# Kernel optimization log

Hardware: AMD Instinct MI355X
Metric: run time of the kernel (lower is better)

The kernel has to match this reference:

```python
import jax, jax.numpy as jnp
import numpy as np

EPS = 1e-8

def _conv(x, w, b=None):
    # NCHW conv, stride 1, SAME padding (k=3, pad=1)
    y = jax.lax.conv_general_dilated(x, w, (1, 1), 'SAME',
                                     dimension_numbers=('NCHW', 'OIHW', 'NCHW'))
    if b is not None:
        y = y + b[None, :, None, None]
    return y

def setup_inputs() -> dict:
    key = jax.random.key(0)
    ks = jax.random.split(key, 6)
    B, C, H, W = 512, 1024, 8, 8
    return {
        'x': jax.random.normal(ks[0], (B, C, H, W), jnp.float32),
        'w1_1': jax.random.normal(ks[1], (1, 1, 3, 3), jnp.float32) * 0.1,
        'w5': jax.random.normal(ks[2], (4, 2, 3, 3), jnp.float32) * 0.1,
        'b5': jax.random.normal(ks[3], (4,), jnp.float32) * 0.1,
        'w6': jax.random.normal(ks[4], (1, 4, 3, 3), jnp.float32) * 0.1,
        'b6': jax.random.normal(ks[5], (1,), jnp.float32) * 0.1,
    }

def reference(x, w1_1, w5, b5, w6, b6):
    B, C, H, W = x.shape  # H == W == 8 by module construction
    m = jnp.max(x, axis=1, keepdims=True)  # [B,1,H,W] channel max
    # 2x2 non-overlapping windows, torch unfold layout -> [B,1,(H/2)*(W/2),4]
    win = m.reshape(B, 1, H // 2, 2, W // 2, 2)
    win = win.transpose(0, 1, 2, 4, 3, 5).reshape(B, 1, (H // 2) * (W // 2), 4)
    # probabilistic pooling: clean inf/nan/negatives, sample per window
    winc = jnp.where(jnp.isinf(win) | jnp.isnan(win) | (win < 0), EPS, win)
    skey = jax.random.key(1)
    idx = jax.random.categorical(skey, winc, axis=-1)  # softmax(winc) multinomial
    mo2 = jnp.take_along_axis(winc, idx[..., None], axis=-1)[..., 0]
    mo2 = mo2.reshape(B, 1, H // 2, W // 2)
    # adaptive max/avg pool (4,4) on 8x8 == 2x2 pooling, reuse windows
    mo3 = win.max(axis=-1).reshape(B, 1, H // 2, W // 2)
    ao4 = win.mean(axis=-1).reshape(B, 1, H // 2, W // 2)
    out2 = 0.1 * mo2 + 0.6 * mo3 + 0.3 * ao4
    out2 = _conv(out2, w1_1)  # bias-free 1->1 conv
    out2 = jax.image.resize(out2, (B, 1, H, W), method='bilinear')  # align_corners=False
    out1 = jnp.concatenate([m, out2], axis=1)  # [B,2,H,W]
    gate = jax.nn.sigmoid(_conv(jax.nn.relu(_conv(out1, w5, b5)), w6, b6))  # [B,1,H,W]
    return jax.nn.relu(x * gate)
```

## Files before the change

kernel.cpp:

```cpp
#include <hip/hip_runtime.h>
#include <math.h>

#define C_DIM 1024
#define HW 64
#define NT 1024
#define F4_PER_BATCH 16384
#define PER_T 16
#define EPSV 1e-8f
#define TINYF 1.17549435e-38f

typedef float f32x4_t __attribute__((ext_vector_type(4)));

__device__ __forceinline__ void keepf(float& v) { asm volatile("" : "+v"(v)); }
__device__ __forceinline__ void keep4(float4& v) {
    keepf(v.x); keepf(v.y); keepf(v.z); keepf(v.w);
}

__device__ __forceinline__ void threefry2x32_01(unsigned x0, unsigned x1,
                                                unsigned& o0, unsigned& o1) {
    const unsigned ks0 = 0u, ks1 = 1u, ks2 = 0x1BD11BDBu;
    x0 += ks0; x1 += ks1;
#define TF_R(r) { x0 += x1; x1 = (x1 << (r)) | (x1 >> (32 - (r))); x1 ^= x0; }
    TF_R(13) TF_R(15) TF_R(26) TF_R(6)
    x0 += ks1; x1 += ks2 + 1u;
    TF_R(17) TF_R(29) TF_R(16) TF_R(24)
    x0 += ks2; x1 += ks0 + 2u;
    TF_R(13) TF_R(15) TF_R(26) TF_R(6)
    x0 += ks0; x1 += ks1 + 3u;
    TF_R(17) TF_R(29) TF_R(16) TF_R(24)
    x0 += ks1; x1 += ks2 + 4u;
    TF_R(13) TF_R(15) TF_R(26) TF_R(6)
    x0 += ks2; x1 += ks0 + 5u;
#undef TF_R
    o0 = x0; o1 = x1;
}

__device__ __forceinline__ unsigned jax_random_bits(unsigned n) {
    unsigned o0, o1;
    threefry2x32_01(0u, n, o0, o1);
    return o0 ^ o1;
}

__device__ __forceinline__ bool bad_val(float v) {
    return ((__float_as_uint(v) & 0x7F800000u) == 0x7F800000u) || (v < 0.0f);
}

__global__ __launch_bounds__(NT) void sa_fused_kernel(
    const float* __restrict__ x,
    const float* __restrict__ w11,
    const float* __restrict__ w5,
    const float* __restrict__ b5,
    const float* __restrict__ w6,
    const float* __restrict__ b6,
    float* __restrict__ out)
{
    const int b = blockIdx.x;
    const int t = threadIdx.x;

    const float4* __restrict__ xb = (const float4*)x + (size_t)b * F4_PER_BATCH;
    float4* __restrict__ ob = (float4*)out + (size_t)b * F4_PER_BATCH;

    __shared__ float4 red[16 * 16];
    __shared__ float sm[64];
    __shared__ float sa16[16];
    __shared__ float sb16[16];
    __shared__ float so2[64];
    __shared__ float shid[4 * 64];
    __shared__ __align__(16) float sgate[64];

    float4 xv[PER_T];
    float4 pm = make_float4(-INFINITY, -INFINITY, -INFINITY, -INFINITY);
#pragma unroll
    for (int i = 0; i < PER_T; ++i) {
        xv[i] = xb[t + NT * i];
        pm.x = fmaxf(pm.x, xv[i].x); pm.y = fmaxf(pm.y, xv[i].y);
        pm.z = fmaxf(pm.z, xv[i].z); pm.w = fmaxf(pm.w, xv[i].w);
    }
#pragma unroll
    for (int i = 0; i < PER_T; ++i) keep4(xv[i]);

#pragma unroll
    for (int off = 16; off <= 32; off <<= 1) {
        pm.x = fmaxf(pm.x, __shfl_xor(pm.x, off, 64));
        pm.y = fmaxf(pm.y, __shfl_xor(pm.y, off, 64));
        pm.z = fmaxf(pm.z, __shfl_xor(pm.z, off, 64));
        pm.w = fmaxf(pm.w, __shfl_xor(pm.w, off, 64));
    }
    const int wv = t >> 6, lane = t & 63;
    if (lane < 16) red[wv * 16 + lane] = pm;
    __syncthreads();

    if (t < 64) {
        {
            int g = t & 15, set = t >> 4;
            float4 a = red[(set * 4 + 0) * 16 + g];
#pragma unroll
            for (int w = 1; w < 4; ++w) {
                float4 o = red[(set * 4 + w) * 16 + g];
                a.x = fmaxf(a.x, o.x); a.y = fmaxf(a.y, o.y);
                a.z = fmaxf(a.z, o.z); a.w = fmaxf(a.w, o.w);
            }
#pragma unroll
            for (int off = 16; off <= 32; off <<= 1) {
                a.x = fmaxf(a.x, __shfl_xor(a.x, off, 64));
                a.y = fmaxf(a.y, __shfl_xor(a.y, off, 64));
                a.z = fmaxf(a.z, __shfl_xor(a.z, off, 64));
                a.w = fmaxf(a.w, __shfl_xor(a.w, off, 64));
            }
            if (t < 16) {
                sm[t * 4 + 0] = a.x; sm[t * 4 + 1] = a.y;
                sm[t * 4 + 2] = a.z; sm[t * 4 + 3] = a.w;
            }
        }
        __builtin_amdgcn_wave_barrier();

        {
            int w = t >> 2, j = t & 3;
            int hh = 2 * (w >> 2) + (j >> 1), ww = 2 * (w & 3) + (j & 1);
            float v = sm[hh * 8 + ww];
            float wc = bad_val(v) ? EPSV : v;
            unsigned bits = jax_random_bits((unsigned)(b * 64 + t));
            float f = __uint_as_float(0x3F800000u | (bits >> 9)) - 1.0f;
            float u = fmaxf(TINYF, f + TINYF);
            float sg = -logf(-logf(u));
            float s = wc + sg;
            int bi = j;
            float bwc = wc;
            float mx = v;
            float ssum = v;
#pragma unroll
            for (int m = 1; m <= 2; m <<= 1) {
                float s2   = __shfl_xor(s, m, 64);
                int   bi2  = __shfl_xor(bi, m, 64);
                float bwc2 = __shfl_xor(bwc, m, 64);
                float mx2  = __shfl_xor(mx, m, 64);
                float ss2  = __shfl_xor(ssum, m, 64);
                bool take = (s2 > s) || (s2 == s && bi2 < bi);
                if (take) { s = s2; bi = bi2; bwc = bwc2; }
                mx = fmaxf(mx, mx2);
                ssum += ss2;
            }
            if (j == 0) sa16[w] = 0.1f * bwc + 0.6f * mx + 0.3f * (ssum * 0.25f);
        }
        __builtin_amdgcn_wave_barrier();

        if (t < 16) {
            int i = t >> 2, j = t & 3;
            float acc = 0.0f;
#pragma unroll
            for (int dy = -1; dy <= 1; ++dy) {
                int yy = i + dy;
                if (yy < 0 || yy > 3) continue;
#pragma unroll
                for (int dx = -1; dx <= 1; ++dx) {
                    int xx = j + dx;
                    if (xx < 0 || xx > 3) continue;
                    acc += sa16[yy * 4 + xx] * w11[(dy + 1) * 3 + (dx + 1)];
                }
            }
            sb16[t] = acc;
        }
        __builtin_amdgcn_wave_barrier();

        {
            int y = t >> 3, xx2 = t & 7;
            float sy = (y + 0.5f) * 0.5f - 0.5f;
            float sx = (xx2 + 0.5f) * 0.5f - 0.5f;
            float fy = fminf(fmaxf(sy, 0.0f), 3.0f);
            float fx = fminf(fmaxf(sx, 0.0f), 3.0f);
            int iy0 = (int)floorf(fy); int iy1 = min(iy0 + 1, 3); float ry = fy - (float)iy0;
            int ix0 = (int)floorf(fx); int ix1 = min(ix0 + 1, 3); float rx = fx - (float)ix0;
            float v00 = sb16[iy0 * 4 + ix0], v01 = sb16[iy0 * 4 + ix1];
            float v10 = sb16[iy1 * 4 + ix0], v11 = sb16[iy1 * 4 + ix1];
            float top = v00 * (1.0f - rx) + v01 * rx;
            float bot = v10 * (1.0f - rx) + v11 * rx;
            so2[t] = top * (1.0f - ry) + bot * ry;
        }
        __builtin_amdgcn_wave_barrier();

        {
            int y = t >> 3, x2 = t & 7;
            float a0 = b5[0], a1 = b5[1], a2 = b5[2], a3 = b5[3];
#pragma unroll
            for (int dy = -1; dy <= 1; ++dy) {
                int yy = y + dy;
                if (yy < 0 || yy > 7) continue;
#pragma unroll
                for (int dx = -1; dx <= 1; ++dx) {
                    int xx = x2 + dx;
                    if (xx < 0 || xx > 7) continue;
                    float i0 = sm[yy * 8 + xx];
                    float i1 = so2[yy * 8 + xx];
                    int kk = (dy + 1) * 3 + (dx + 1);
                    a0 += i0 * w5[0 * 18 + kk] + i1 * w5[0 * 18 + 9 + kk];
                    a1 += i0 * w5[1 * 18 + kk] + i1 * w5[1 * 18 + 9 + kk];
                    a2 += i0 * w5[2 * 18 + kk] + i1 * w5[2 * 18 + 9 + kk];
                    a3 += i0 * w5[3 * 18 + kk] + i1 * w5[3 * 18 + 9 + kk];
                }
            }
            shid[0 * 64 + t] = fmaxf(a0, 0.0f);
            shid[1 * 64 + t] = fmaxf(a1, 0.0f);
            shid[2 * 64 + t] = fmaxf(a2, 0.0f);
            shid[3 * 64 + t] = fmaxf(a3, 0.0f);
        }
        __builtin_amdgcn_wave_barrier();

        {
            int y = t >> 3, x2 = t & 7;
            float acc = b6[0];
#pragma unroll
            for (int dy = -1; dy <= 1; ++dy) {
                int yy = y + dy;
                if (yy < 0 || yy > 7) continue;
#pragma unroll
                for (int dx = -1; dx <= 1; ++dx) {
                    int xx = x2 + dx;
                    if (xx < 0 || xx > 7) continue;
                    int kk = (dy + 1) * 3 + (dx + 1);
                    int p = yy * 8 + xx;
                    acc += shid[0 * 64 + p] * w6[0 + kk]
                         + shid[1 * 64 + p] * w6[9 + kk]
                         + shid[2 * 64 + p] * w6[18 + kk]
                         + shid[3 * 64 + p] * w6[27 + kk];
                }
            }
            sgate[t] = 1.0f / (1.0f + expf(-acc));
        }
    }
    __syncthreads();

    const float4 gv = ((const float4*)sgate)[t & 15];
#pragma unroll
    for (int i = 0; i < PER_T; ++i) {
        float4 v = xv[i];
        f32x4_t o;
        o.x = fmaxf(v.x * gv.x, 0.0f);
        o.y = fmaxf(v.y * gv.y, 0.0f);
        o.z = fmaxf(v.z * gv.z, 0.0f);
        o.w = fmaxf(v.w * gv.w, 0.0f);
        __builtin_nontemporal_store(o, (f32x4_t*)&ob[t + NT * i]);
    }
}

extern "C" void kernel_launch(void* const* d_in, const int* in_sizes, int n_in,
                              void* d_out, int out_size, void* d_ws, size_t ws_size,
                              hipStream_t stream) {
    const float* x   = (const float*)d_in[0];
    const float* w11 = (const float*)d_in[1];
    const float* w5  = (const float*)d_in[2];
    const float* b5  = (const float*)d_in[3];
    const float* w6  = (const float*)d_in[4];
    const float* b6  = (const float*)d_in[5];
    float* out  = (float*)d_out;

    int B = in_sizes[0] / (C_DIM * HW);
    sa_fused_kernel<<<dim3(B), dim3(NT), 0, stream>>>(x, w11, w5, b5, w6, b6, out);
}
```

Measured before the change: 243.2 us.

## Process two batches per block and overlap second load with first gate network

Each block now handles two batch items. The second batch's 64 KB load and its Gumbel noise generation are issued while the first batch's small gate network runs, and the first batch's Gumbel noise is computed while its own loads are in flight. In the write phase, x is reloaded from global memory (likely an L2 hit) instead of being held in registers, which cuts register pressure but adds reads. The grid is halved to B/2 blocks, which lowers parallelism and assumes B is even.

```diff
diff --git a/kernel.cpp b/kernel.cpp
--- a/kernel.cpp
+++ b/kernel.cpp
@@ -4,17 +4,14 @@
 #define C_DIM 1024
 #define HW 64
 #define NT 1024
-#define F4_PER_BATCH 16384
+#define F4B 16384
 #define PER_T 16
 #define EPSV 1e-8f
 #define TINYF 1.17549435e-38f
 
 typedef float f32x4_t __attribute__((ext_vector_type(4)));
 
-__device__ __forceinline__ void keepf(float& v) { asm volatile("" : "+v"(v)); }
-__device__ __forceinline__ void keep4(float4& v) {
-    keepf(v.x); keepf(v.y); keepf(v.z); keepf(v.w);
-}
+__device__ __forceinline__ void keepf(float v) { asm volatile("" :: "v"(v)); }
 
 __device__ __forceinline__ void threefry2x32_01(unsigned x0, unsigned x1,
                                                 unsigned& o0, unsigned& o1) {
@@ -41,8 +38,157 @@
     return o0 ^ o1;
 }
 
+__device__ __forceinline__ float gumbel01(unsigned n) {
+    unsigned bits = jax_random_bits(n);
+    float f = __uint_as_float(0x3F800000u | (bits >> 9)) - 1.0f;
+    float u = fmaxf(TINYF, f + TINYF);
+    return -logf(-logf(u));
+}
+
 __device__ __forceinline__ bool bad_val(float v) {
     return ((__float_as_uint(v) & 0x7F800000u) == 0x7F800000u) || (v < 0.0f);
+}
+
+__device__ __forceinline__ void middle_net(
+    int t, float sgum,
+    const float4* __restrict__ red,
+    const float* __restrict__ w11, const float* __restrict__ w5,
+    const float* __restrict__ b5, const float* __restrict__ w6,
+    const float* __restrict__ b6,
+    float* sm, float* sa16, float* sb16, float* so2, float* shid,
+    float* sgate)
+{
+    {
+        int g = t & 15, set = t >> 4;
+        float4 a = red[(set * 4 + 0) * 16 + g];
+#pragma unroll
+        for (int w = 1; w < 4; ++w) {
+            float4 o = red[(set * 4 + w) * 16 + g];
+            a.x = fmaxf(a.x, o.x); a.y = fmaxf(a.y, o.y);
+            a.z = fmaxf(a.z, o.z); a.w = fmaxf(a.w, o.w);
+        }
+#pragma unroll
+        for (int off = 16; off <= 32; off <<= 1) {
+            a.x = fmaxf(a.x, __shfl_xor(a.x, off, 64));
+            a.y = fmaxf(a.y, __shfl_xor(a.y, off, 64));
+            a.z = fmaxf(a.z, __shfl_xor(a.z, off, 64));
+            a.w = fmaxf(a.w, __shfl_xor(a.w, off, 64));
+        }
+        if (t < 16) {
+            sm[t * 4 + 0] = a.x; sm[t * 4 + 1] = a.y;
+            sm[t * 4 + 2] = a.z; sm[t * 4 + 3] = a.w;
+        }
+    }
+    __builtin_amdgcn_wave_barrier();
+
+    {
+        int w = t >> 2, j = t & 3;
+        int hh = 2 * (w >> 2) + (j >> 1), ww = 2 * (w & 3) + (j & 1);
+        float v = sm[hh * 8 + ww];
+        float wc = bad_val(v) ? EPSV : v;
+        float s = wc + sgum;
+        int bi = j;
+        float bwc = wc;
+        float mx = v;
+        float ssum = v;
+#pragma unroll
+        for (int m = 1; m <= 2; m <<= 1) {
+            float s2   = __shfl_xor(s, m, 64);
+            int   bi2  = __shfl_xor(bi, m, 64);
+            float bwc2 = __shfl_xor(bwc, m, 64);
+            float mx2  = __shfl_xor(mx, m, 64);
+            float ss2  = __shfl_xor(ssum, m, 64);
+            bool take = (s2 > s) || (s2 == s && bi2 < bi);
+            if (take) { s = s2; bi = bi2; bwc = bwc2; }
+            mx = fmaxf(mx, mx2);
+            ssum += ss2;
+        }
+        if (j == 0) sa16[w] = 0.1f * bwc + 0.6f * mx + 0.3f * (ssum * 0.25f);
+    }
+    __builtin_amdgcn_wave_barrier();
+
+    if (t < 16) {
+        int i = t >> 2, j = t & 3;
+        float acc = 0.0f;
+#pragma unroll
+        for (int dy = -1; dy <= 1; ++dy) {
+            int yy = i + dy;
+            if (yy < 0 || yy > 3) continue;
+#pragma unroll
+            for (int dx = -1; dx <= 1; ++dx) {
+                int xx = j + dx;
+                if (xx < 0 || xx > 3) continue;
+                acc += sa16[yy * 4 + xx] * w11[(dy + 1) * 3 + (dx + 1)];
+            }
+        }
+        sb16[t] = acc;
+    }
+    __builtin_amdgcn_wave_barrier();
+
+    {
+        int y = t >> 3, xx2 = t & 7;
+        float sy = (y + 0.5f) * 0.5f - 0.5f;
+        float sx = (xx2 + 0.5f) * 0.5f - 0.5f;
+        float fy = fminf(fmaxf(sy, 0.0f), 3.0f);
+        float fx = fminf(fmaxf(sx, 0.0f), 3.0f);
+        int iy0 = (int)floorf(fy); int iy1 = min(iy0 + 1, 3); float ry = fy - (float)iy0;
+        int ix0 = (int)floorf(fx); int ix1 = min(ix0 + 1, 3); float rx = fx - (float)ix0;
+        float v00 = sb16[iy0 * 4 + ix0], v01 = sb16[iy0 * 4 + ix1];
+        float v10 = sb16[iy1 * 4 + ix0], v11 = sb16[iy1 * 4 + ix1];
+        float top = v00 * (1.0f - rx) + v01 * rx;
+        float bot = v10 * (1.0f - rx) + v11 * rx;
+        so2[t] = top * (1.0f - ry) + bot * ry;
+    }
+    __builtin_amdgcn_wave_barrier();
+
+    {
+        int y = t >> 3, x2 = t & 7;
+        float a0 = b5[0], a1 = b5[1], a2 = b5[2], a3 = b5[3];
+#pragma unroll
+        for (int dy = -1; dy <= 1; ++dy) {
+            int yy = y + dy;
+            if (yy < 0 || yy > 7) continue;
+#pragma unroll
+            for (int dx = -1; dx <= 1; ++dx) {
+                int xx = x2 + dx;
+                if (xx < 0 || xx > 7) continue;
+                float i0 = sm[yy * 8 + xx];
+                float i1 = so2[yy * 8 + xx];
+                int kk = (dy + 1) * 3 + (dx + 1);
+                a0 += i0 * w5[0 * 18 + kk] + i1 * w5[0 * 18 + 9 + kk];
+                a1 += i0 * w5[1 * 18 + kk] + i1 * w5[1 * 18 + 9 + kk];
+                a2 += i0 * w5[2 * 18 + kk] + i1 * w5[2 * 18 + 9 + kk];
+                a3 += i0 * w5[3 * 18 + kk] + i1 * w5[3 * 18 + 9 + kk];
+            }
+        }
+        shid[0 * 64 + t] = fmaxf(a0, 0.0f);
+        shid[1 * 64 + t] = fmaxf(a1, 0.0f);
+        shid[2 * 64 + t] = fmaxf(a2, 0.0f);
+        shid[3 * 64 + t] = fmaxf(a3, 0.0f);
+    }
+    __builtin_amdgcn_wave_barrier();
+
+    {
+        int y = t >> 3, x2 = t & 7;
+        float acc = b6[0];
+#pragma unroll
+        for (int dy = -1; dy <= 1; ++dy) {
+            int yy = y + dy;
+            if (yy < 0 || yy > 7) continue;
+#pragma unroll
+            for (int dx = -1; dx <= 1; ++dx) {
+                int xx = x2 + dx;
+                if (xx < 0 || xx > 7) continue;
+                int kk = (dy + 1) * 3 + (dx + 1);
+                int p = yy * 8 + xx;
+                acc += shid[0 * 64 + p] * w6[0 + kk]
+                     + shid[1 * 64 + p] * w6[9 + kk]
+                     + shid[2 * 64 + p] * w6[18 + kk]
+                     + shid[3 * 64 + p] * w6[27 + kk];
+            }
+        }
+        sgate[t] = 1.0f / (1.0f + expf(-acc));
+    }
 }
 
 __global__ __launch_bounds__(NT) void sa_fused_kernel(
@@ -54,31 +200,38 @@
     const float* __restrict__ b6,
     float* __restrict__ out)
 {
-    const int b = blockIdx.x;
+    const int bid = blockIdx.x;
     const int t = threadIdx.x;
-
-    const float4* __restrict__ xb = (const float4*)x + (size_t)b * F4_PER_BATCH;
-    float4* __restrict__ ob = (float4*)out + (size_t)b * F4_PER_BATCH;
-
-    __shared__ float4 red[16 * 16];
-    __shared__ float sm[64];
-    __shared__ float sa16[16];
-    __shared__ float sb16[16];
-    __shared__ float so2[64];
-    __shared__ float shid[4 * 64];
-    __shared__ __align__(16) float sgate[64];
+    const int half = gridDim.x;
+    const int b0 = bid, b1 = bid + half;
+    const int wv = t >> 6, lane = t & 63;
+
+    const float4* __restrict__ x4 = (const float4*)x;
+    const float4* __restrict__ xb0 = x4 + (size_t)b0 * F4B;
+    const float4* __restrict__ xb1 = x4 + (size_t)b1 * F4B;
+    float4* __restrict__ ob0 = (float4*)out + (size_t)b0 * F4B;
+    float4* __restrict__ ob1 = (float4*)out + (size_t)b1 * F4B;
+
+    __shared__ float4 red0[16 * 16];
+    __shared__ float4 red1[16 * 16];
+    __shared__ float sm[64], sa16[16], sb16[16], so2[64], shid[4 * 64];
+    __shared__ __align__(16) float sgate0[64];
+    __shared__ __align__(16) float sgate1[64];
 
     float4 xv[PER_T];
+#pragma unroll
+    for (int i = 0; i < PER_T; ++i) xv[i] = xb0[t + NT * i];
+    if (t == 0) {
+        keepf(w11[0]); keepf(w5[0]); keepf(w5[32]); keepf(w5[64]);
+        keepf(b5[0]);  keepf(w6[0]); keepf(w6[32]); keepf(b6[0]);
+    }
+    const float sgum0 = gumbel01((unsigned)(b0 * 64 + lane));
     float4 pm = make_float4(-INFINITY, -INFINITY, -INFINITY, -INFINITY);
 #pragma unroll
     for (int i = 0; i < PER_T; ++i) {
-        xv[i] = xb[t + NT * i];
         pm.x = fmaxf(pm.x, xv[i].x); pm.y = fmaxf(pm.y, xv[i].y);
         pm.z = fmaxf(pm.z, xv[i].z); pm.w = fmaxf(pm.w, xv[i].w);
     }
-#pragma unroll
-    for (int i = 0; i < PER_T; ++i) keep4(xv[i]);
-
 #pragma unroll
     for (int off = 16; off <= 32; off <<= 1) {
         pm.x = fmaxf(pm.x, __shfl_xor(pm.x, off, 64));
@@ -86,159 +239,62 @@
         pm.z = fmaxf(pm.z, __shfl_xor(pm.z, off, 64));
         pm.w = fmaxf(pm.w, __shfl_xor(pm.w, off, 64));
     }
-    const int wv = t >> 6, lane = t & 63;
-    if (lane < 16) red[wv * 16 + lane] = pm;
+    if (lane < 16) red0[wv * 16 + lane] = pm;
     __syncthreads();
 
-    if (t < 64) {
-        {
-            int g = t & 15, set = t >> 4;
-            float4 a = red[(set * 4 + 0) * 16 + g];
-#pragma unroll
-            for (int w = 1; w < 4; ++w) {
-                float4 o = red[(set * 4 + w) * 16 + g];
-                a.x = fmaxf(a.x, o.x); a.y = fmaxf(a.y, o.y);
-                a.z = fmaxf(a.z, o.z); a.w = fmaxf(a.w, o.w);
-            }
-#pragma unroll
-            for (int off = 16; off <= 32; off <<= 1) {
-                a.x = fmaxf(a.x, __shfl_xor(a.x, off, 64));
-                a.y = fmaxf(a.y, __shfl_xor(a.y, off, 64));
-                a.z = fmaxf(a.z, __shfl_xor(a.z, off, 64));
-                a.w = fmaxf(a.w, __shfl_xor(a.w, off, 64));
-            }
-            if (t < 16) {
-                sm[t * 4 + 0] = a.x; sm[t * 4 + 1] = a.y;
-                sm[t * 4 + 2] = a.z; sm[t * 4 + 3] = a.w;
-            }
-        }
-        __builtin_amdgcn_wave_barrier();
-
-        {
-            int w = t >> 2, j = t & 3;
-            int hh = 2 * (w >> 2) + (j >> 1), ww = 2 * (w & 3) + (j & 1);
-            float v = sm[hh * 8 + ww];
-            float wc = bad_val(v) ? EPSV : v;
-            unsigned bits = jax_random_bits((unsigned)(b * 64 + t));
-            float f = __uint_as_float(0x3F800000u | (bits >> 9)) - 1.0f;
-            float u = fmaxf(TINYF, f + TINYF);
-            float sg = -logf(-logf(u));
-            float s = wc + sg;
-            int bi = j;
-            float bwc = wc;
-            float mx = v;
-            float ssum = v;
-#pragma unroll
-            for (int m = 1; m <= 2; m <<= 1) {
-                float s2   = __shfl_xor(s, m, 64);
-                int   bi2  = __shfl_xor(bi, m, 64);
-                float bwc2 = __shfl_xor(bwc, m, 64);
-                float mx2  = __shfl_xor(mx, m, 64);
-                float ss2  = __shfl_xor(ssum, m, 64);
-                bool take = (s2 > s) || (s2 == s && bi2 < bi);
-                if (take) { s = s2; bi = bi2; bwc = bwc2; }
-                mx = fmaxf(mx, mx2);
-                ssum += ss2;
-            }
-            if (j == 0) sa16[w] = 0.1f * bwc + 0.6f * mx + 0.3f * (ssum * 0.25f);
-        }
-        __builtin_amdgcn_wave_barrier();
-
-        if (t < 16) {
-            int i = t >> 2, j = t & 3;
-            float acc = 0.0f;
-#pragma unroll
-            for (int dy = -1; dy <= 1; ++dy) {
-                int yy = i + dy;
-                if (yy < 0 || yy > 3) continue;
-#pragma unroll
-                for (int dx = -1; dx <= 1; ++dx) {
-                    int xx = j + dx;
-                    if (xx < 0 || xx > 3) continue;
-                    acc += sa16[yy * 4 + xx] * w11[(dy + 1) * 3 + (dx + 1)];
-                }
-            }
-            sb16[t] = acc;
-        }
-        __builtin_amdgcn_wave_barrier();
-
-        {
-            int y = t >> 3, xx2 = t & 7;
-            float sy = (y + 0.5f) * 0.5f - 0.5f;
-            float sx = (xx2 + 0.5f) * 0.5f - 0.5f;
-            float fy = fminf(fmaxf(sy, 0.0f), 3.0f);
-            float fx = fminf(fmaxf(sx, 0.0f), 3.0f);
-            int iy0 = (int)floorf(fy); int iy1 = min(iy0 + 1, 3); float ry = fy - (float)iy0;
-            int ix0 = (int)floorf(fx); int ix1 = min(ix0 + 1, 3); float rx = fx - (float)ix0;
-            float v00 = sb16[iy0 * 4 + ix0], v01 = sb16[iy0 * 4 + ix1];
-            float v10 = sb16[iy1 * 4 + ix0], v11 = sb16[iy1 * 4 + ix1];
-            float top = v00 * (1.0f - rx) + v01 * rx;
-            float bot = v10 * (1.0f - rx) + v11 * rx;
-            so2[t] = top * (1.0f - ry) + bot * ry;
-        }
-        __builtin_amdgcn_wave_barrier();
-
-        {
-            int y = t >> 3, x2 = t & 7;
-            float a0 = b5[0], a1 = b5[1], a2 = b5[2], a3 = b5[3];
-#pragma unroll
-            for (int dy = -1; dy <= 1; ++dy) {
-                int yy = y + dy;
-                if (yy < 0 || yy > 7) continue;
-#pragma unroll
-                for (int dx = -1; dx <= 1; ++dx) {
-                    int xx = x2 + dx;
-                    if (xx < 0 || xx > 7) continue;
-                    float i0 = sm[yy * 8 + xx];
-                    float i1 = so2[yy * 8 + xx];
-                    int kk = (dy + 1) * 3 + (dx + 1);
-                    a0 += i0 * w5[0 * 18 + kk] + i1 * w5[0 * 18 + 9 + kk];
-                    a1 += i0 * w5[1 * 18 + kk] + i1 * w5[1 * 18 + 9 + kk];
-                    a2 += i0 * w5[2 * 18 + kk] + i1 * w5[2 * 18 + 9 + kk];
-                    a3 += i0 * w5[3 * 18 + kk] + i1 * w5[3 * 18 + 9 + kk];
-                }
-            }
-            shid[0 * 64 + t] = fmaxf(a0, 0.0f);
-            shid[1 * 64 + t] = fmaxf(a1, 0.0f);
-            shid[2 * 64 + t] = fmaxf(a2, 0.0f);
-            shid[3 * 64 + t] = fmaxf(a3, 0.0f);
-        }
-        __builtin_amdgcn_wave_barrier();
-
-        {
-            int y = t >> 3, x2 = t & 7;
-            float acc = b6[0];
-#pragma unroll
-            for (int dy = -1; dy <= 1; ++dy) {
-                int yy = y + dy;
-                if (yy < 0 || yy > 7) continue;
-#pragma unroll
-                for (int dx = -1; dx <= 1; ++dx) {
-                    int xx = x2 + dx;
-                    if (xx < 0 || xx > 7) continue;
-                    int kk = (dy + 1) * 3 + (dx + 1);
-                    int p = yy * 8 + xx;
-                    acc += shid[0 * 64 + p] * w6[0 + kk]
-                         + shid[1 * 64 + p] * w6[9 + kk]
-                         + shid[2 * 64 + p] * w6[18 + kk]
-                         + shid[3 * 64 + p] * w6[27 + kk];
-                }
-            }
-            sgate[t] = 1.0f / (1.0f + expf(-acc));
-        }
-    }
+    float4 yv[PER_T];
+#pragma unroll
+    for (int i = 0; i < PER_T; ++i) yv[i] = xb1[t + NT * i];
+    const float sgum1 = gumbel01((unsigned)(b1 * 64 + lane));
+    if (t < 64)
+        middle_net(t, sgum0, red0, w11, w5, b5, w6, b6,
+                   sm, sa16, sb16, so2, shid, sgate0);
+    pm = make_float4(-INFINITY, -INFINITY, -INFINITY, -INFINITY);
+#pragma unroll
+    for (int i = 0; i < PER_T; ++i) {
+        pm.x = fmaxf(pm.x, yv[i].x); pm.y = fmaxf(pm.y, yv[i].y);
+        pm.z = fmaxf(pm.z, yv[i].z); pm.w = fmaxf(pm.w, yv[i].w);
+    }
+#pragma unroll
+    for (int off = 16; off <= 32; off <<= 1) {
+        pm.x = fmaxf(pm.x, __shfl_xor(pm.x, off, 64));
+        pm.y = fmaxf(pm.y, __shfl_xor(pm.y, off, 64));
+        pm.z = fmaxf(pm.z, __shfl_xor(pm.z, off, 64));
+        pm.w = fmaxf(pm.w, __shfl_xor(pm.w, off, 64));
+    }
+    if (lane < 16) red1[wv * 16 + lane] = pm;
     __syncthreads();
 
-    const float4 gv = ((const float4*)sgate)[t & 15];
-#pragma unroll
-    for (int i = 0; i < PER_T; ++i) {
-        float4 v = xv[i];
-        f32x4_t o;
-        o.x = fmaxf(v.x * gv.x, 0.0f);
-        o.y = fmaxf(v.y * gv.y, 0.0f);
-        o.z = fmaxf(v.z * gv.z, 0.0f);
-        o.w = fmaxf(v.w * gv.w, 0.0f);
-        __builtin_nontemporal_store(o, (f32x4_t*)&ob[t + NT * i]);
+    if (t < 64)
+        middle_net(t, sgum1, red1, w11, w5, b5, w6, b6,
+                   sm, sa16, sb16, so2, shid, sgate1);
+    {
+        const float4 g0 = ((const float4*)sgate0)[t & 15];
+#pragma unroll
+        for (int i = 0; i < PER_T; ++i) {
+            float4 v = xb0[t + NT * i];
+            f32x4_t o;
+            o.x = fmaxf(v.x * g0.x, 0.0f);
+            o.y = fmaxf(v.y * g0.y, 0.0f);
+            o.z = fmaxf(v.z * g0.z, 0.0f);
+            o.w = fmaxf(v.w * g0.w, 0.0f);
+            __builtin_nontemporal_store(o, (f32x4_t*)&ob0[t + NT * i]);
+        }
+    }
+    __syncthreads();
+
+    {
+        const float4 g1 = ((const float4*)sgate1)[t & 15];
+#pragma unroll
+        for (int i = 0; i < PER_T; ++i) {
+            float4 v = xb1[t + NT * i];
+            f32x4_t o;
+            o.x = fmaxf(v.x * g1.x, 0.0f);
+            o.y = fmaxf(v.y * g1.y, 0.0f);
+            o.z = fmaxf(v.z * g1.z, 0.0f);
+            o.w = fmaxf(v.w * g1.w, 0.0f);
+            __builtin_nontemporal_store(o, (f32x4_t*)&ob1[t + NT * i]);
+        }
     }
 }
 
@@ -254,5 +310,5 @@
     float* out  = (float*)d_out;
 
     int B = in_sizes[0] / (C_DIM * HW);
-    sa_fused_kernel<<<dim3(B), dim3(NT), 0, stream>>>(x, w11, w5, b5, w6, b6, out);
-}
+    sa_fused_kernel<<<dim3(B / 2), dim3(NT), 0, stream>>>(x, w11, w5, b5, w6, b6, out);
+}
```

After: 263.9 us. 8.5% more time.

## Stop holding the batch in registers; reload x from cache for the gating pass

Applied to the files above, without the earlier changes.

Changes the block to 512 threads with 32 float4 per thread and no longer keeps the 256 KB batch slice in registers. The second pass re-reads x from global memory, relying on the cache, and the launch bounds now ask for more resident blocks to raise occupancy. Gumbel noise generation is hoisted before the wave barrier so it can overlap with the reduction. This trades register pressure for a second read of x, which may hit L2/MALL or may cost extra HBM traffic.

```diff
diff --git a/kernel.cpp b/kernel.cpp
--- a/kernel.cpp
+++ b/kernel.cpp
@@ -3,18 +3,13 @@
 
 #define C_DIM 1024
 #define HW 64
-#define NT 1024
-#define F4_PER_BATCH 16384
-#define PER_T 16
+#define NT 512
+#define F4B 16384
+#define PER_T 32
 #define EPSV 1e-8f
 #define TINYF 1.17549435e-38f
 
 typedef float f32x4_t __attribute__((ext_vector_type(4)));
-
-__device__ __forceinline__ void keepf(float& v) { asm volatile("" : "+v"(v)); }
-__device__ __forceinline__ void keep4(float4& v) {
-    keepf(v.x); keepf(v.y); keepf(v.z); keepf(v.w);
-}
 
 __device__ __forceinline__ void threefry2x32_01(unsigned x0, unsigned x1,
                                                 unsigned& o0, unsigned& o1) {
@@ -41,11 +36,18 @@
     return o0 ^ o1;
 }
 
+__device__ __forceinline__ float gumbel01(unsigned n) {
+    unsigned bits = jax_random_bits(n);
+    float f = __uint_as_float(0x3F800000u | (bits >> 9)) - 1.0f;
+    float u = fmaxf(TINYF, f + TINYF);
+    return -logf(-logf(u));
+}
+
 __device__ __forceinline__ bool bad_val(float v) {
     return ((__float_as_uint(v) & 0x7F800000u) == 0x7F800000u) || (v < 0.0f);
 }
 
-__global__ __launch_bounds__(NT) void sa_fused_kernel(
+__global__ __launch_bounds__(NT, 4) void sa_fused_kernel(
     const float* __restrict__ x,
     const float* __restrict__ w11,
     const float* __restrict__ w5,
@@ -57,28 +59,20 @@
     const int b = blockIdx.x;
     const int t = threadIdx.x;
 
-    const float4* __restrict__ xb = (const float4*)x + (size_t)b * F4_PER_BATCH;
-    float4* __restrict__ ob = (float4*)out + (size_t)b * F4_PER_BATCH;
-
-    __shared__ float4 red[16 * 16];
-    __shared__ float sm[64];
-    __shared__ float sa16[16];
-    __shared__ float sb16[16];
-    __shared__ float so2[64];
-    __shared__ float shid[4 * 64];
+    const float4* __restrict__ xb = (const float4*)x + (size_t)b * F4B;
+    float4* __restrict__ ob = (float4*)out + (size_t)b * F4B;
+
+    __shared__ float4 red[8 * 16];
+    __shared__ float sm[64], sa16[16], sb16[16], so2[64], shid[4 * 64];
     __shared__ __align__(16) float sgate[64];
 
-    float4 xv[PER_T];
     float4 pm = make_float4(-INFINITY, -INFINITY, -INFINITY, -INFINITY);
 #pragma unroll
     for (int i = 0; i < PER_T; ++i) {
-        xv[i] = xb[t + NT * i];
-        pm.x = fmaxf(pm.x, xv[i].x); pm.y = fmaxf(pm.y, xv[i].y);
-        pm.z = fmaxf(pm.z, xv[i].z); pm.w = fmaxf(pm.w, xv[i].w);
-    }
-#pragma unroll
-    for (int i = 0; i < PER_T; ++i) keep4(xv[i]);
-
+        float4 v = xb[t + NT * i];
+        pm.x = fmaxf(pm.x, v.x); pm.y = fmaxf(pm.y, v.y);
+        pm.z = fmaxf(pm.z, v.z); pm.w = fmaxf(pm.w, v.w);
+    }
 #pragma unroll
     for (int off = 16; off <= 32; off <<= 1) {
         pm.x = fmaxf(pm.x, __shfl_xor(pm.x, off, 64));
@@ -93,13 +87,10 @@
     if (t < 64) {
         {
             int g = t & 15, set = t >> 4;
-            float4 a = red[(set * 4 + 0) * 16 + g];
-#pragma unroll
-            for (int w = 1; w < 4; ++w) {
-                float4 o = red[(set * 4 + w) * 16 + g];
-                a.x = fmaxf(a.x, o.x); a.y = fmaxf(a.y, o.y);
-                a.z = fmaxf(a.z, o.z); a.w = fmaxf(a.w, o.w);
-            }
+            float4 a = red[(set * 2 + 0) * 16 + g];
+            float4 o = red[(set * 2 + 1) * 16 + g];
+            a.x = fmaxf(a.x, o.x); a.y = fmaxf(a.y, o.y);
+            a.z = fmaxf(a.z, o.z); a.w = fmaxf(a.w, o.w);
 #pragma unroll
             for (int off = 16; off <= 32; off <<= 1) {
                 a.x = fmaxf(a.x, __shfl_xor(a.x, off, 64));
@@ -112,6 +103,7 @@
                 sm[t * 4 + 2] = a.z; sm[t * 4 + 3] = a.w;
             }
         }
+        const float sgum = gumbel01((unsigned)(b * 64 + t));
         __builtin_amdgcn_wave_barrier();
 
         {
@@ -119,22 +111,18 @@
             int hh = 2 * (w >> 2) + (j >> 1), ww = 2 * (w & 3) + (j & 1);
             float v = sm[hh * 8 + ww];
             float wc = bad_val(v) ? EPSV : v;
-            unsigned bits = jax_random_bits((unsigned)(b * 64 + t));
-            float f = __uint_as_float(0x3F800000u | (bits >> 9)) - 1.0f;
-            float u = fmaxf(TINYF, f + TINYF);
-            float sg = -logf(-logf(u));
-            float s = wc + sg;
+            float s = wc + sgum;
             int bi = j;
             float bwc = wc;
             float mx = v;
             float ssum = v;
 #pragma unroll
-            for (int m = 1; m <= 2; m <<= 1) {
-                float s2   = __shfl_xor(s, m, 64);
-                int   bi2  = __shfl_xor(bi, m, 64);
-                float bwc2 = __shfl_xor(bwc, m, 64);
-                float mx2  = __shfl_xor(mx, m, 64);
-                float ss2  = __shfl_xor(ssum, m, 64);
+            for (int mk = 1; mk <= 2; mk <<= 1) {
+                float s2   = __shfl_xor(s, mk, 64);
+                int   bi2  = __shfl_xor(bi, mk, 64);
+                float bwc2 = __shfl_xor(bwc, mk, 64);
+                float mx2  = __shfl_xor(mx, mk, 64);
+                float ss2  = __shfl_xor(ssum, mk, 64);
                 bool take = (s2 > s) || (s2 == s && bi2 < bi);
                 if (take) { s = s2; bi = bi2; bwc = bwc2; }
                 mx = fmaxf(mx, mx2);
@@ -232,7 +220,7 @@
     const float4 gv = ((const float4*)sgate)[t & 15];
 #pragma unroll
     for (int i = 0; i < PER_T; ++i) {
-        float4 v = xv[i];
+        float4 v = xb[t + NT * i];
         f32x4_t o;
         o.x = fmaxf(v.x * gv.x, 0.0f);
         o.y = fmaxf(v.y * gv.y, 0.0f);
```

Result: slower. 250.6 us (+3.0%).
